# Kernel tuning notes

Measured on AMD Instinct MI355X. Metric: run time of the kernel, lower is better.

## Reference

```python
import jax, jax.numpy as jnp
import numpy as np
import math

B, TH, STEPS = 4, 120, 8
D_IN, D_MODEL, N_HEADS, N_LAYERS, D_FF = 32, 512, 8, 4, 2048
N_SUB = 5
D_HEAD = D_MODEL // N_HEADS
EPS = 1e-5


def _pos_encoding(T, d):
    pos = jnp.arange(T, dtype=jnp.float32)[:, None]
    div = jnp.exp(jnp.arange(0, d, 2, dtype=jnp.float32) * (-math.log(10000.0) / d))
    pe = jnp.zeros((T, d), dtype=jnp.float32)
    pe = pe.at[:, 0::2].set(jnp.sin(pos * div))
    pe = pe.at[:, 1::2].set(jnp.cos(pos * div))
    return pe


def setup_inputs() -> dict:
    key = jax.random.key(0)
    ks = jax.random.split(key, 16)
    s = 0.02
    n = lambda k, shp: jax.random.normal(k, shp, jnp.float32) * s
    return {
        "history": jax.random.normal(ks[0], (B, TH, D_IN), jnp.float32),
        "steps": STEPS,
        "W_emb": n(ks[1], (D_MODEL, D_IN)),
        "b_emb": jnp.zeros((D_MODEL,), jnp.float32),
        "Wq": n(ks[2], (N_LAYERS, D_MODEL, D_MODEL)),
        "Wk": n(ks[3], (N_LAYERS, D_MODEL, D_MODEL)),
        "Wv": n(ks[4], (N_LAYERS, D_MODEL, D_MODEL)),
        "Wo": n(ks[5], (N_LAYERS, D_MODEL, D_MODEL)),
        "ln1_g": jnp.ones((N_LAYERS, D_MODEL), jnp.float32),
        "ln1_b": jnp.zeros((N_LAYERS, D_MODEL), jnp.float32),
        "W1": n(ks[6], (N_LAYERS, D_FF, D_MODEL)),
        "b1": jnp.zeros((N_LAYERS, D_FF), jnp.float32),
        "W2": n(ks[7], (N_LAYERS, D_MODEL, D_FF)),
        "b2": jnp.zeros((N_LAYERS, D_MODEL), jnp.float32),
        "ln2_g": jnp.ones((N_LAYERS, D_MODEL), jnp.float32),
        "ln2_b": jnp.zeros((N_LAYERS, D_MODEL), jnp.float32),
        "Wr1": n(ks[8], (D_FF, 2 * D_MODEL)),
        "br1": jnp.zeros((D_FF,), jnp.float32),
        "Wr2": n(ks[9], (D_IN, D_FF)),
        "br2": jnp.zeros((D_IN,), jnp.float32),
    }


def _layernorm(x, g, b):
    mu = x.mean(-1, keepdims=True)
    var = ((x - mu) ** 2).mean(-1, keepdims=True)
    return (x - mu) / jnp.sqrt(var + EPS) * g + b


def reference(history, steps, W_emb, b_emb, Wq, Wk, Wv, Wo, ln1_g, ln1_b,
              W1, b1, W2, b2, ln2_g, ln2_b, Wr1, br1, Wr2, br2):
    total_len = TH + steps
    pe = _pos_encoding(total_len, D_MODEL)
    idx = jnp.arange(total_len)
    # NOTE: faithful to source: mask True where kv index > q index (equinox: True = attend)
    mask = idx[:, None] < idx[None, :]
    neg = jnp.finfo(jnp.float32).min
    scale = math.sqrt(D_MODEL)

    def transformer(buf):  # buf: [T, D_IN] -> [T, D_MODEL]
        h = (buf @ W_emb.T + b_emb) * scale + pe
        for l in range(N_LAYERS):
            q = (h @ Wq[l].T).reshape(total_len, N_HEADS, D_HEAD)
            k = (h @ Wk[l].T).reshape(total_len, N_HEADS, D_HEAD)
            v = (h @ Wv[l].T).reshape(total_len, N_HEADS, D_HEAD)
            logits = jnp.einsum("qhd,khd->hqk", q, k) / math.sqrt(D_HEAD)
            logits = jnp.where(mask[None], logits, neg)
            w = jax.nn.softmax(logits, axis=-1)
            attn = jnp.einsum("hqk,khd->qhd", w, v).reshape(total_len, D_MODEL)
            h = _layernorm(h + attn @ Wo[l].T, ln1_g[l], ln1_b[l])
            m = jax.nn.gelu(h @ W1[l].T + b1[l]) @ W2[l].T + b2[l]
            h = _layernorm(h + m, ln2_g[l], ln2_b[l])
        return h

    def refine(start_val, ctx):  # start_val: [D_IN], ctx: [D_MODEL]
        def body(i, cur):
            we = (W_emb @ cur + b_emb) * scale
            comb = jnp.concatenate([we, ctx])
            delta = Wr2 @ jax.nn.gelu(Wr1 @ comb + br1) + br2
            return cur + delta
        return jax.lax.fori_loop(0, N_SUB, body, start_val)

    def single(hist):  # [TH, D_IN] -> [steps, D_IN]
        buf = jnp.zeros((total_len, D_IN), jnp.float32).at[:TH].set(hist)

        def scan_fn(buf, step_idx):
            h = transformer(buf)  # full recompute each decode step (no KV cache)
            ptr = TH + step_idx
            next_val = refine(buf[ptr - 1], h[ptr - 1])
            return buf.at[ptr].set(next_val), next_val

        _, preds = jax.lax.scan(scan_fn, buf, jnp.arange(steps))
        return preds

    return jax.vmap(single)(history)
```

## Files before the change

kernel.cpp:

```cpp
#include <hip/hip_runtime.h>
#include <math.h>

namespace {
constexpr int NB = 4;
constexpr int SEQ = 128;
constexpr int TH_ = 120;
constexpr int NSTEP = 8;
constexpr int DMODEL = 512;
constexpr int NHEAD = 8;
constexpr int DHEAD = 64;
constexpr int DFFN = 2048;
constexpr int DIN = 32;
constexpr int MROWS = NB*SEQ;
constexpr float SCALE_EMB = 22.627416997969522f;
constexpr float LN_EPS = 1e-5f;
constexpr float NEGF = -3.4028234663852886e38f;
constexpr float PE_C = -0.017988946039015984f;
}

using short8 = __attribute__((ext_vector_type(8))) short;
using f32x4  = __attribute__((ext_vector_type(4))) float;

__device__ __forceinline__ float wave_sum(float v){
#pragma unroll
  for(int off=32;off;off>>=1) v += __shfl_xor(v,off,64);
  return v;
}
__device__ __forceinline__ float blk_sum(float v, float* scr){
  v = wave_sum(v);
  __syncthreads();
  if((threadIdx.x&63)==0) scr[threadIdx.x>>6]=v;
  __syncthreads();
  return scr[0]+scr[1]+scr[2]+scr[3];
}
__device__ __forceinline__ float gelu_t(float x){
  float t = 0.7978845608028654f*(x + 0.044715f*x*x*x);
  return 0.5f*x*(1.0f + tanhf(t));
}
__device__ __forceinline__ float pe_val(int t, int d){
  float div = expf((float)(d & ~1) * PE_C);
  float a = (float)t * div;
  return (d & 1) ? cosf(a) : sinf(a);
}
__device__ __forceinline__ unsigned short f2b(float f){
  union { float f; unsigned u; } c; c.f = f;
  unsigned u = c.u + 0x7FFFu + ((c.u>>16)&1u);
  return (unsigned short)(u>>16);
}
__device__ __forceinline__ short8 pack8(const float* f){
  short8 s;
#pragma unroll
  for(int i=0;i<8;i++) s[i] = (short)f2b(f[i]);
  return s;
}

__global__ __launch_bounds__(256) void conv_w(const float* __restrict__ Wq,
                                              const float* __restrict__ Wk,
                                              const float* __restrict__ Wv,
                                              const float* __restrict__ Wo,
                                              const float* __restrict__ W1,
                                              const float* __restrict__ W2,
                                              unsigned short* __restrict__ dst){
  size_t base = ((size_t)blockIdx.x*256 + threadIdx.x)*8;
  if(base >= 12582912u) return;
  const float* src; size_t off;
  if(base < 1048576u){ src=Wq; off=base; }
  else if(base < 2097152u){ src=Wk; off=base-1048576u; }
  else if(base < 3145728u){ src=Wv; off=base-2097152u; }
  else if(base < 4194304u){ src=Wo; off=base-3145728u; }
  else if(base < 8388608u){ src=W1; off=base-4194304u; }
  else { src=W2; off=base-8388608u; }
  float4 a = *(const float4*)(src+off);
  float4 b = *(const float4*)(src+off+4);
  float f[8] = {a.x,a.y,a.z,a.w,b.x,b.y,b.z,b.w};
  *(short8*)(dst + base) = pack8(f);
}

__global__ __launch_bounds__(256) void init_h0(const float* __restrict__ hist,
                                               const float* __restrict__ W_emb,
                                               const float* __restrict__ b_emb,
                                               float* __restrict__ h0,
                                               unsigned short* __restrict__ h0b){
  int bt = blockIdx.x;
  int b = bt >> 7, t = bt & 127;
  __shared__ float x[DIN];
  if(threadIdx.x < DIN)
    x[threadIdx.x] = (t < TH_) ? hist[((size_t)b*TH_ + t)*DIN + threadIdx.x] : 0.f;
  __syncthreads();
  for(int d = threadIdx.x; d < DMODEL; d += 256){
    float s = 0.f;
#pragma unroll 8
    for(int i=0;i<DIN;i++) s += W_emb[d*DIN+i]*x[i];
    float v = SCALE_EMB*(s + b_emb[d]) + pe_val(t,d);
    h0[(size_t)bt*DMODEL + d] = v;
    h0b[(size_t)bt*DMODEL + d] = f2b(v);
  }
}

__global__ __launch_bounds__(256) void init_misc(const float* __restrict__ Wr1,
                                                 const float* __restrict__ W_emb,
                                                 const float* __restrict__ b_emb,
                                                 const float* __restrict__ br1,
                                                 const float* __restrict__ hist,
                                                 float* __restrict__ M1,
                                                 float* __restrict__ cb1,
                                                 float* __restrict__ cur_x){
  __shared__ float row[DMODEL];
  int j0 = blockIdx.x*8;
  for(int jj=0;jj<8;jj++){
    int j = j0+jj;
    for(int k=threadIdx.x;k<DMODEL;k+=256) row[k] = Wr1[(size_t)j*1024 + k];
    __syncthreads();
    if(threadIdx.x < DIN){
      int i = threadIdx.x; float s = 0.f;
      for(int k=0;k<DMODEL;k++) s += row[k]*W_emb[k*DIN+i];
      M1[j*DIN+i] = SCALE_EMB*s;
    } else if(threadIdx.x == DIN){
      float s=0.f;
      for(int k=0;k<DMODEL;k++) s += row[k]*b_emb[k];
      cb1[j] = br1[j] + SCALE_EMB*s;
    }
    __syncthreads();
  }
  if(blockIdx.x==0 && threadIdx.x<NB*DIN){
    int b = threadIdx.x>>5, i = threadIdx.x&31;
    cur_x[b*DIN+i] = hist[((size_t)b*TH_ + (TH_-1))*DIN + i];
  }
}

__global__ __launch_bounds__(256) void lnpass(const float* __restrict__ X,
                                              const float* __restrict__ g,
                                              const float* __restrict__ bta,
                                              float* __restrict__ Y,
                                              unsigned short* __restrict__ Yb){
  int row = blockIdx.x*4 + (threadIdx.x>>6);
  int l = threadIdx.x&63;
  const float* xp = X + (size_t)row*DMODEL + l*8;
  float4 x0 = *(const float4*)xp;
  float4 x1 = *(const float4*)(xp+4);
  float f[8] = {x0.x,x0.y,x0.z,x0.w,x1.x,x1.y,x1.z,x1.w};
  float s = 0.f;
#pragma unroll
  for(int i=0;i<8;i++) s += f[i];
  s = wave_sum(s);
  float mu = s*(1.f/DMODEL);
  float v = 0.f;
#pragma unroll
  for(int i=0;i<8;i++){ float d0=f[i]-mu; v += d0*d0; }
  v = wave_sum(v);
  float rs = rsqrtf(v*(1.f/DMODEL) + LN_EPS);
#pragma unroll
  for(int i=0;i<8;i++){
    int c = l*8+i;
    f[i] = (f[i]-mu)*rs*g[c] + bta[c];
  }
  float* yp = Y + (size_t)row*DMODEL + l*8;
  *(float4*)yp     = make_float4(f[0],f[1],f[2],f[3]);
  *(float4*)(yp+4) = make_float4(f[4],f[5],f[6],f[7]);
  *(short8*)(Yb + (size_t)row*DMODEL + l*8) = pack8(f);
}

__global__ __launch_bounds__(256) void gemm_bf(
    const unsigned short* __restrict__ A16, int Ka,
    const unsigned short* __restrict__ Wa,
    const unsigned short* __restrict__ Wb,
    const unsigned short* __restrict__ Wc,
    const float* __restrict__ bias, const float* __restrict__ resid,
    float* __restrict__ Cf, unsigned short* __restrict__ Cb,
    int c_rs, int c_mode, int act)
{
  int n0 = blockIdx.x*128;
  int m0 = blockIdx.y*64;
  int tid = threadIdx.x, w = tid>>6, ln = tid&63;
  __shared__ __align__(16) unsigned short As[64][72];
  __shared__ __align__(16) unsigned short Bs[128][72];

  const unsigned short* Wsrc; int nrow0;
  if(c_mode==2){ int which = n0>>9; Wsrc = (which==0?Wa:(which==1?Wb:Wc)); nrow0 = n0&511; }
  else { Wsrc = Wa; nrow0 = n0; }

  f32x4 acc[4][2];
#pragma unroll
  for(int i=0;i<4;i++)
#pragma unroll
    for(int j=0;j<2;j++) acc[i][j] = (f32x4){0.f,0.f,0.f,0.f};

  int fr = ln&15, fq = (ln>>4)*8;
  int arow = tid>>2, akq = (tid&3)*16;
  int brow = tid>>1, bkq = (tid&1)*32;

  for(int k0=0;k0<Ka;k0+=64){
    const unsigned short* ap = A16 + (size_t)(m0+arow)*Ka + k0 + akq;
    short8 a0 = *(const short8*)ap;
    short8 a1 = *(const short8*)(ap+8);
    const unsigned short* bp = Wsrc + (size_t)(nrow0+brow)*Ka + k0 + bkq;
    short8 b0 = *(const short8*)bp;
    short8 b1 = *(const short8*)(bp+8);
    short8 b2 = *(const short8*)(bp+16);
    short8 b3 = *(const short8*)(bp+24);
    *(short8*)&As[arow][akq]   = a0;
    *(short8*)&As[arow][akq+8] = a1;
    *(short8*)&Bs[brow][bkq]    = b0;
    *(short8*)&Bs[brow][bkq+8]  = b1;
    *(short8*)&Bs[brow][bkq+16] = b2;
    *(short8*)&Bs[brow][bkq+24] = b3;
    __syncthreads();
    short8 af[4][2], bf[2][2];
#pragma unroll
    for(int kf=0;kf<2;kf++){
#pragma unroll
      for(int rt=0;rt<4;rt++) af[rt][kf] = *(const short8*)&As[rt*16 + fr][kf*32 + fq];
#pragma unroll
      for(int ct=0;ct<2;ct++) bf[ct][kf] = *(const short8*)&Bs[32*w + ct*16 + fr][kf*32 + fq];
    }
#pragma unroll
    for(int kf=0;kf<2;kf++)
#pragma unroll
      for(int rt=0;rt<4;rt++)
#pragma unroll
        for(int ct=0;ct<2;ct++)
          acc[rt][ct] = __builtin_amdgcn_mfma_f32_16x16x32_bf16(af[rt][kf], bf[ct][kf], acc[rt][ct], 0, 0, 0);
    __syncthreads();
  }

#pragma unroll
  for(int rt=0;rt<4;rt++){
#pragma unroll
    for(int ct=0;ct<2;ct++){
      int n = n0 + 32*w + ct*16 + fr;
#pragma unroll
      for(int r=0;r<4;r++){
        int row = m0 + rt*16 + (ln>>4)*4 + r;
        float v = acc[rt][ct][r];
        if(bias)  v += bias[n];
        if(resid) v += resid[(size_t)row*DMODEL + n];
        if(act==1) v = gelu_t(v);
        if(c_mode==0)      Cf[(size_t)row*c_rs + n] = v;
        else if(c_mode==1) Cb[(size_t)row*c_rs + n] = f2b(v);
        else {
          int which = n>>9, rem = n&511;
          int b = row>>7, t = row&127;
          Cf[(size_t)which*(MROWS*DMODEL) +
             ((size_t)(b*NHEAD + (rem>>6))*SEQ + t)*DHEAD + (rem&63)] = v;
        }
      }
    }
  }
}

__global__ __launch_bounds__(256) void attn_k(const float* __restrict__ qb,
                                              const float* __restrict__ kb,
                                              const float* __restrict__ vb,
                                              unsigned short* __restrict__ attb){
  int b = blockIdx.z, h = blockIdx.y;
  int r0 = blockIdx.x*32;
  const float* Kh = kb + (size_t)(b*NHEAD+h)*SEQ*DHEAD;
  const float* Vh = vb + (size_t)(b*NHEAD+h)*SEQ*DHEAD;
  const float* Qh = qb + (size_t)(b*NHEAD+h)*SEQ*DHEAD;
  __shared__ float kv[SEQ][DHEAD];
  __shared__ float wsm[32][132];
  __shared__ float qs[32][68];
  int tid = threadIdx.x;
  int d = tid&63, rr = tid>>6;

  for(int k=rr;k<SEQ;k+=4) kv[k][d ^ (k&60)] = Kh[k*DHEAD + d];
  for(int r=rr;r<32;r+=4)  qs[r][d] = Qh[(size_t)(r0+r)*DHEAD + d];
  __syncthreads();

  {
    int rp = tid>>4;
    int kg = tid&15;
    float acc[2][8];
#pragma unroll
    for(int i=0;i<2;i++)
#pragma unroll
      for(int kk=0;kk<8;kk++) acc[i][kk]=0.f;
#pragma unroll 4
    for(int d4=0;d4<16;d4++){
      float4 q0 = *(const float4*)&qs[2*rp][d4*4];
      float4 q1 = *(const float4*)&qs[2*rp+1][d4*4];
#pragma unroll
      for(int kk=0;kk<8;kk++){
        int k = 8*kg + kk;
        int off = (d4*4) ^ (k&60);
        float4 kv4 = *(const float4*)&kv[k][off];
        acc[0][kk] += q0.x*kv4.x + q0.y*kv4.y + q0.z*kv4.z + q0.w*kv4.w;
        acc[1][kk] += q1.x*kv4.x + q1.y*kv4.y + q1.z*kv4.z + q1.w*kv4.w;
      }
    }
#pragma unroll
    for(int i=0;i<2;i++){
      int t = r0 + 2*rp + i;
#pragma unroll
      for(int kk=0;kk<8;kk++){
        int k = 8*kg + kk;
        wsm[2*rp+i][k] = (k > t) ? acc[i][kk]*0.125f : NEGF;
      }
    }
  }
  __syncthreads();

  {
    int l2 = tid&63, wv = tid>>6;
    for(int r=wv;r<32;r+=4){
      float l0 = wsm[r][l2], l1 = wsm[r][l2+64];
      float m = fmaxf(l0,l1);
#pragma unroll
      for(int off=32;off;off>>=1) m = fmaxf(m, __shfl_xor(m,off,64));
      float e0 = expf(l0-m), e1 = expf(l1-m);
      float s = e0+e1;
      s = wave_sum(s);
      float inv = 1.f/s;
      wsm[r][l2] = e0*inv; wsm[r][l2+64] = e1*inv;
    }
  }
  __syncthreads();

  for(int k=rr;k<SEQ;k+=4) kv[k][d] = Vh[k*DHEAD + d];
  __syncthreads();

  {
    int dq = (tid&15)*4, rg = tid>>4;
    for(int r=rg;r<32;r+=16){
      float4 acc2 = make_float4(0.f,0.f,0.f,0.f);
      for(int k=0;k<SEQ;k++){
        float w0 = wsm[r][k];
        float4 v = *(const float4*)&kv[k][dq];
        acc2.x += w0*v.x; acc2.y += w0*v.y; acc2.z += w0*v.z; acc2.w += w0*v.w;
      }
      int row = b*SEQ + r0 + r;
      unsigned short* op = attb + (size_t)row*DMODEL + h*DHEAD + dq;
      op[0]=f2b(acc2.x); op[1]=f2b(acc2.y); op[2]=f2b(acc2.z); op[3]=f2b(acc2.w);
    }
  }
}

__global__ __launch_bounds__(256) void ctx_k(const float* __restrict__ r2,
                                             const float* __restrict__ g2,
                                             const float* __restrict__ b2,
                                             const float* __restrict__ Wr1,
                                             const float* __restrict__ cb1,
                                             float* __restrict__ ctxt, int ptr){
  int b = blockIdx.y; int j0 = blockIdx.x*128;
  __shared__ float raw[DMODEL], ctx[DMODEL], scr[4];
  int tid = threadIdx.x;
  const float* rp = r2 + (size_t)(b*SEQ + ptr-1)*DMODEL;
  for(int k=tid;k<DMODEL;k+=256) raw[k]=rp[k];
  __syncthreads();
  float s = 0.f;
  for(int k=tid;k<DMODEL;k+=256) s += raw[k];
  s = blk_sum(s, scr);
  float mu = s/(float)DMODEL;
  float v = 0.f;
  for(int k=tid;k<DMODEL;k+=256){ float d0 = raw[k]-mu; v += d0*d0; }
  v = blk_sum(v, scr);
  float rs = rsqrtf(v/(float)DMODEL + LN_EPS);
  for(int k=tid;k<DMODEL;k+=256) ctx[k] = (raw[k]-mu)*rs*g2[k] + b2[k];
  __syncthreads();
  int wv = tid>>6, l2 = tid&63;
  for(int jj=wv;jj<128;jj+=4){
    int j = j0+jj;
    const float* wp = Wr1 + (size_t)j*1024 + 512;
    float acc = 0.f;
#pragma unroll
    for(int q=0;q<8;q++){ int k = l2 + 64*q; acc += wp[k]*ctx[k]; }
    acc = wave_sum(acc);
    if(l2==0) ctxt[b*DFFN + j] = acc + cb1[j];
  }
}

__global__ __launch_bounds__(256) void refine_fin(const float* __restrict__ M1,
                                                  const float* __restrict__ ctxt,
                                                  const float* __restrict__ Wr2,
                                                  const float* __restrict__ br2,
                                                  float* __restrict__ cur_x,
                                                  const float* __restrict__ W_emb,
                                                  const float* __restrict__ b_emb,
                                                  float* __restrict__ out,
                                                  float* __restrict__ h0,
                                                  unsigned short* __restrict__ h0b,
                                                  int s, int ptr){
  int b = blockIdx.x, tid = threadIdx.x;
  __shared__ float cur[DIN], gs[DFFN], dscr[DIN];
  if(tid < DIN) cur[tid] = cur_x[b*DIN + tid];
  __syncthreads();
  for(int sub=0; sub<5; sub++){
    for(int jj=tid; jj<DFFN; jj+=256){
      float u = ctxt[b*DFFN + jj];
      const float* mp = M1 + (size_t)jj*DIN;
#pragma unroll
      for(int p=0;p<8;p++){
        float4 mv = *(const float4*)(mp + 4*p);
        u += mv.x*cur[4*p] + mv.y*cur[4*p+1] + mv.z*cur[4*p+2] + mv.w*cur[4*p+3];
      }
      gs[jj] = gelu_t(u);
    }
    __syncthreads();
    int w = tid>>6, l = tid&63;
#pragma unroll
    for(int q=0;q<8;q++){
      int i = w*8 + q;
      const float* wr = Wr2 + (size_t)i*DFFN;
      float a = 0.f;
#pragma unroll
      for(int p=0;p<8;p++){
        int j0 = p*256 + l*4;
        float4 wv = *(const float4*)(wr + j0);
        float4 gv = *(const float4*)&gs[j0];
        a += wv.x*gv.x + wv.y*gv.y + wv.z*gv.z + wv.w*gv.w;
      }
      a = wave_sum(a);
      if(l==0) dscr[i] = a;
    }
    __syncthreads();
    if(tid < DIN) cur[tid] += dscr[tid] + br2[tid];
    __syncthreads();
  }
  if(tid < DIN){
    out[(b*NSTEP + s)*DIN + tid] = cur[tid];
    cur_x[b*DIN + tid] = cur[tid];
  }
  __syncthreads();
  for(int d=tid; d<DMODEL; d+=256){
    float s2 = 0.f;
#pragma unroll 8
    for(int i=0;i<DIN;i++) s2 += W_emb[d*DIN+i]*cur[i];
    float v = SCALE_EMB*(s2 + b_emb[d]) + pe_val(ptr, d);
    size_t idx = (size_t)(b*SEQ + ptr)*DMODEL + d;
    h0[idx] = v;
    h0b[idx] = f2b(v);
  }
}

extern "C" void kernel_launch(void* const* d_in, const int* in_sizes, int n_in,
                              void* d_out, int out_size, void* d_ws, size_t ws_size,
                              hipStream_t stream) {
  (void)in_sizes; (void)n_in; (void)out_size; (void)ws_size;
  const float* hist = (const float*)d_in[0];
  const float* W_emb= (const float*)d_in[2];
  const float* b_emb= (const float*)d_in[3];
  const float* Wq   = (const float*)d_in[4];
  const float* Wk   = (const float*)d_in[5];
  const float* Wv   = (const float*)d_in[6];
  const float* Wo   = (const float*)d_in[7];
  const float* ln1g = (const float*)d_in[8];
  const float* ln1b = (const float*)d_in[9];
  const float* W1   = (const float*)d_in[10];
  const float* b1   = (const float*)d_in[11];
  const float* W2   = (const float*)d_in[12];
  const float* b2v  = (const float*)d_in[13];
  const float* ln2g = (const float*)d_in[14];
  const float* ln2b = (const float*)d_in[15];
  const float* Wr1  = (const float*)d_in[16];
  const float* br1  = (const float*)d_in[17];
  const float* Wr2  = (const float*)d_in[18];
  const float* br2  = (const float*)d_in[19];
  float* out = (float*)d_out;
  float* ws  = (float*)d_ws;

  const size_t BTD = (size_t)MROWS*DMODEL;
  const size_t BTDH = BTD/2;
  float* h0   = ws;
  unsigned short* h0b = (unsigned short*)(h0 + BTD);
  float* r2   = h0 + BTD + BTDH;
  float* hln  = r2 + BTD;
  float* hp   = hln + BTD;
  unsigned short* hpb = (unsigned short*)(hp + BTD);
  float* qb   = hp + BTD + BTDH;
  float* kb   = qb + BTD;
  float* vb   = kb + BTD;
  unsigned short* attb = (unsigned short*)(vb + BTD);
  unsigned short* hlnb = (unsigned short*)(vb + BTD + BTDH);
  unsigned short* fbuf16 = (unsigned short*)qb;
  float* r1   = qb;
  unsigned short* W16 = (unsigned short*)(qb + 4*BTD);
  float* after_w = qb + 4*BTD + 6291456;
  float* M1   = after_w;
  float* cb1  = M1 + (size_t)DFFN*DIN;
  float* ctxt = cb1 + DFFN;
  float* cur_x= ctxt + NB*DFFN;

  unsigned short* Wq16 = W16;
  unsigned short* Wk16 = W16 + 1048576;
  unsigned short* Wv16 = W16 + 2097152;
  unsigned short* Wo16 = W16 + 3145728;
  unsigned short* W116 = W16 + 4194304;
  unsigned short* W216 = W16 + 8388608;

  conv_w<<<dim3(6144),dim3(256),0,stream>>>(Wq,Wk,Wv,Wo,W1,W2,W16);
  init_h0<<<dim3(MROWS),dim3(256),0,stream>>>(hist,W_emb,b_emb,h0,h0b);
  init_misc<<<dim3(256),dim3(256),0,stream>>>(Wr1,W_emb,b_emb,br1,hist,M1,cb1,cur_x);

  for(int s=0;s<NSTEP;s++){
    int ptr = TH_ + s;
    for(int l=0;l<4;l++){
      if(l>0)
        lnpass<<<dim3(128),dim3(256),0,stream>>>(r2, ln2g+(l-1)*DMODEL, ln2b+(l-1)*DMODEL, hln, hlnb);
      const unsigned short* A16 = (l==0)? h0b : hlnb;
      const float* res1 = (l==0)? h0 : hln;

      gemm_bf<<<dim3(12,8),dim3(256),0,stream>>>(A16, DMODEL,
          Wq16 + (size_t)l*262144, Wk16 + (size_t)l*262144, Wv16 + (size_t)l*262144,
          nullptr, nullptr, qb, nullptr, 0, 2, 0);

      attn_k<<<dim3(4,NHEAD,NB),dim3(256),0,stream>>>(qb,kb,vb,attb);

      gemm_bf<<<dim3(4,8),dim3(256),0,stream>>>(attb, DMODEL,
          Wo16 + (size_t)l*262144, nullptr, nullptr,
          nullptr, res1, r1, nullptr, DMODEL, 0, 0);

      lnpass<<<dim3(128),dim3(256),0,stream>>>(r1, ln1g+l*DMODEL, ln1b+l*DMODEL, hp, hpb);

      gemm_bf<<<dim3(16,8),dim3(256),0,stream>>>(hpb, DMODEL,
          W116 + (size_t)l*1048576, nullptr, nullptr,
          b1 + l*DFFN, nullptr, nullptr, fbuf16, DFFN, 1, 1);

      gemm_bf<<<dim3(4,8),dim3(256),0,stream>>>(fbuf16, DFFN,
          W216 + (size_t)l*1048576, nullptr, nullptr,
          b2v + l*DMODEL, hp, r2, nullptr, DMODEL, 0, 0);
    }

    ctx_k<<<dim3(16,NB),dim3(256),0,stream>>>(r2, ln2g + 3*DMODEL, ln2b + 3*DMODEL,
                                              Wr1, cb1, ctxt, ptr);
    refine_fin<<<dim3(NB),dim3(256),0,stream>>>(M1, ctxt, Wr2, br2, cur_x,
                                                W_emb, b_emb, out, h0, h0b, s, ptr);
  }
}
```

Measured before the change: 4.746 ms.

## Fuse per-step decode kernels into one persistent kernel with grid barriers

Replaces the roughly 230 small kernel launches of the decode loop with a single persistent 128-block kernel. Stages are separated by an atomic-counter grid barrier, and the stage bodies share one shared-memory union. The aim is to remove launch overhead and inter-kernel gaps. In exchange, every stage runs on at most 128 blocks, so some stages leave blocks idle, and the spin barrier assumes all blocks are co-resident.

```diff
diff --git a/kernel.cpp b/kernel.cpp
--- a/kernel.cpp
+++ b/kernel.cpp
@@ -16,10 +16,13 @@
 constexpr float LN_EPS = 1e-5f;
 constexpr float NEGF = -3.4028234663852886e38f;
 constexpr float PE_C = -0.017988946039015984f;
+constexpr unsigned NBLK = 128;
 }
 
 using short8 = __attribute__((ext_vector_type(8))) short;
 using f32x4  = __attribute__((ext_vector_type(4))) float;
+
+__device__ unsigned g_cnt = 0;
 
 __device__ __forceinline__ float wave_sum(float v){
 #pragma unroll
@@ -53,6 +56,23 @@
   for(int i=0;i<8;i++) s[i] = (short)f2b(f[i]);
   return s;
 }
+
+__device__ __forceinline__ void gsync(unsigned target){
+  __syncthreads();
+  if(threadIdx.x==0){
+    __hip_atomic_fetch_add(&g_cnt, 1u, __ATOMIC_ACQ_REL, __HIP_MEMORY_SCOPE_AGENT);
+    while(__hip_atomic_load(&g_cnt, __ATOMIC_ACQUIRE, __HIP_MEMORY_SCOPE_AGENT) < target){
+      __builtin_amdgcn_s_sleep(1);
+    }
+  }
+  __syncthreads();
+}
+
+struct SmemG { unsigned short As[64][72]; unsigned short Bs[128][72]; };
+struct SmemA { float kv[SEQ][DHEAD]; float wsm[32][132]; float qs[32][68]; };
+struct SmemC { float raw[DMODEL]; float ctx[DMODEL]; float scr[4]; };
+struct SmemR { float cur[DIN]; float gs[DFFN]; float dscr[DIN]; };
+union alignas(16) SmemU { SmemG g; SmemA a; SmemC c; SmemR r; };
 
 __global__ __launch_bounds__(256) void conv_w(const float* __restrict__ Wq,
                                               const float* __restrict__ Wk,
@@ -105,6 +125,7 @@
                                                  float* __restrict__ M1,
                                                  float* __restrict__ cb1,
                                                  float* __restrict__ cur_x){
+  if(blockIdx.x==0 && threadIdx.x==255) g_cnt = 0u;
   __shared__ float row[DMODEL];
   int j0 = blockIdx.x*8;
   for(int jj=0;jj<8;jj++){
@@ -128,12 +149,14 @@
   }
 }
 
-__global__ __launch_bounds__(256) void lnpass(const float* __restrict__ X,
-                                              const float* __restrict__ g,
-                                              const float* __restrict__ bta,
-                                              float* __restrict__ Y,
-                                              unsigned short* __restrict__ Yb){
-  int row = blockIdx.x*4 + (threadIdx.x>>6);
+
+__device__ __forceinline__ void lnpass_body(int vb,
+                                            const float* __restrict__ X,
+                                            const float* __restrict__ g,
+                                            const float* __restrict__ bta,
+                                            float* __restrict__ Y,
+                                            unsigned short* __restrict__ Yb){
+  int row = vb*4 + (threadIdx.x>>6);
   int l = threadIdx.x&63;
   const float* xp = X + (size_t)row*DMODEL + l*8;
   float4 x0 = *(const float4*)xp;
@@ -160,7 +183,7 @@
   *(short8*)(Yb + (size_t)row*DMODEL + l*8) = pack8(f);
 }
 
-__global__ __launch_bounds__(256) void gemm_bf(
+__device__ __forceinline__ void gemm_body(int bx, int by, SmemG& S,
     const unsigned short* __restrict__ A16, int Ka,
     const unsigned short* __restrict__ Wa,
     const unsigned short* __restrict__ Wb,
@@ -169,11 +192,9 @@
     float* __restrict__ Cf, unsigned short* __restrict__ Cb,
     int c_rs, int c_mode, int act)
 {
-  int n0 = blockIdx.x*128;
-  int m0 = blockIdx.y*64;
+  int n0 = bx*128;
+  int m0 = by*64;
   int tid = threadIdx.x, w = tid>>6, ln = tid&63;
-  __shared__ __align__(16) unsigned short As[64][72];
-  __shared__ __align__(16) unsigned short Bs[128][72];
 
   const unsigned short* Wsrc; int nrow0;
   if(c_mode==2){ int which = n0>>9; Wsrc = (which==0?Wa:(which==1?Wb:Wc)); nrow0 = n0&511; }
@@ -198,20 +219,20 @@
     short8 b1 = *(const short8*)(bp+8);
     short8 b2 = *(const short8*)(bp+16);
     short8 b3 = *(const short8*)(bp+24);
-    *(short8*)&As[arow][akq]   = a0;
-    *(short8*)&As[arow][akq+8] = a1;
-    *(short8*)&Bs[brow][bkq]    = b0;
-    *(short8*)&Bs[brow][bkq+8]  = b1;
-    *(short8*)&Bs[brow][bkq+16] = b2;
-    *(short8*)&Bs[brow][bkq+24] = b3;
+    *(short8*)&S.As[arow][akq]   = a0;
+    *(short8*)&S.As[arow][akq+8] = a1;
+    *(short8*)&S.Bs[brow][bkq]    = b0;
+    *(short8*)&S.Bs[brow][bkq+8]  = b1;
+    *(short8*)&S.Bs[brow][bkq+16] = b2;
+    *(short8*)&S.Bs[brow][bkq+24] = b3;
     __syncthreads();
     short8 af[4][2], bf[2][2];
 #pragma unroll
     for(int kf=0;kf<2;kf++){
 #pragma unroll
-      for(int rt=0;rt<4;rt++) af[rt][kf] = *(const short8*)&As[rt*16 + fr][kf*32 + fq];
-#pragma unroll
-      for(int ct=0;ct<2;ct++) bf[ct][kf] = *(const short8*)&Bs[32*w + ct*16 + fr][kf*32 + fq];
+      for(int rt=0;rt<4;rt++) af[rt][kf] = *(const short8*)&S.As[rt*16 + fr][kf*32 + fq];
+#pragma unroll
+      for(int ct=0;ct<2;ct++) bf[ct][kf] = *(const short8*)&S.Bs[32*w + ct*16 + fr][kf*32 + fq];
     }
 #pragma unroll
     for(int kf=0;kf<2;kf++)
@@ -248,23 +269,20 @@
   }
 }
 
-__global__ __launch_bounds__(256) void attn_k(const float* __restrict__ qb,
-                                              const float* __restrict__ kb,
-                                              const float* __restrict__ vb,
-                                              unsigned short* __restrict__ attb){
-  int b = blockIdx.z, h = blockIdx.y;
-  int r0 = blockIdx.x*32;
-  const float* Kh = kb + (size_t)(b*NHEAD+h)*SEQ*DHEAD;
-  const float* Vh = vb + (size_t)(b*NHEAD+h)*SEQ*DHEAD;
-  const float* Qh = qb + (size_t)(b*NHEAD+h)*SEQ*DHEAD;
-  __shared__ float kv[SEQ][DHEAD];
-  __shared__ float wsm[32][132];
-  __shared__ float qs[32][68];
+__device__ __forceinline__ void attn_body(int bx, int h, int b, SmemA& S,
+                                          const float* __restrict__ qb,
+                                          const float* __restrict__ kb,
+                                          const float* __restrict__ vbuf,
+                                          unsigned short* __restrict__ attb){
+  int r0 = bx*32;
+  const float* Kh = kb   + (size_t)(b*NHEAD+h)*SEQ*DHEAD;
+  const float* Vh = vbuf + (size_t)(b*NHEAD+h)*SEQ*DHEAD;
+  const float* Qh = qb   + (size_t)(b*NHEAD+h)*SEQ*DHEAD;
   int tid = threadIdx.x;
   int d = tid&63, rr = tid>>6;
 
-  for(int k=rr;k<SEQ;k+=4) kv[k][d ^ (k&60)] = Kh[k*DHEAD + d];
-  for(int r=rr;r<32;r+=4)  qs[r][d] = Qh[(size_t)(r0+r)*DHEAD + d];
+  for(int k=rr;k<SEQ;k+=4) S.kv[k][d ^ (k&60)] = Kh[k*DHEAD + d];
+  for(int r=rr;r<32;r+=4)  S.qs[r][d] = Qh[(size_t)(r0+r)*DHEAD + d];
   __syncthreads();
 
   {
@@ -277,13 +295,13 @@
       for(int kk=0;kk<8;kk++) acc[i][kk]=0.f;
 #pragma unroll 4
     for(int d4=0;d4<16;d4++){
-      float4 q0 = *(const float4*)&qs[2*rp][d4*4];
-      float4 q1 = *(const float4*)&qs[2*rp+1][d4*4];
+      float4 q0 = *(const float4*)&S.qs[2*rp][d4*4];
+      float4 q1 = *(const float4*)&S.qs[2*rp+1][d4*4];
 #pragma unroll
       for(int kk=0;kk<8;kk++){
         int k = 8*kg + kk;
         int off = (d4*4) ^ (k&60);
-        float4 kv4 = *(const float4*)&kv[k][off];
+        float4 kv4 = *(const float4*)&S.kv[k][off];
         acc[0][kk] += q0.x*kv4.x + q0.y*kv4.y + q0.z*kv4.z + q0.w*kv4.w;
         acc[1][kk] += q1.x*kv4.x + q1.y*kv4.y + q1.z*kv4.z + q1.w*kv4.w;
       }
@@ -294,7 +312,7 @@
 #pragma unroll
       for(int kk=0;kk<8;kk++){
         int k = 8*kg + kk;
-        wsm[2*rp+i][k] = (k > t) ? acc[i][kk]*0.125f : NEGF;
+        S.wsm[2*rp+i][k] = (k > t) ? acc[i][kk]*0.125f : NEGF;
       }
     }
   }
@@ -303,7 +321,7 @@
   {
     int l2 = tid&63, wv = tid>>6;
     for(int r=wv;r<32;r+=4){
-      float l0 = wsm[r][l2], l1 = wsm[r][l2+64];
+      float l0 = S.wsm[r][l2], l1 = S.wsm[r][l2+64];
       float m = fmaxf(l0,l1);
 #pragma unroll
       for(int off=32;off;off>>=1) m = fmaxf(m, __shfl_xor(m,off,64));
@@ -311,12 +329,12 @@
       float s = e0+e1;
       s = wave_sum(s);
       float inv = 1.f/s;
-      wsm[r][l2] = e0*inv; wsm[r][l2+64] = e1*inv;
-    }
-  }
-  __syncthreads();
-
-  for(int k=rr;k<SEQ;k+=4) kv[k][d] = Vh[k*DHEAD + d];
+      S.wsm[r][l2] = e0*inv; S.wsm[r][l2+64] = e1*inv;
+    }
+  }
+  __syncthreads();
+
+  for(int k=rr;k<SEQ;k+=4) S.kv[k][d] = Vh[k*DHEAD + d];
   __syncthreads();
 
   {
@@ -324,8 +342,8 @@
     for(int r=rg;r<32;r+=16){
       float4 acc2 = make_float4(0.f,0.f,0.f,0.f);
       for(int k=0;k<SEQ;k++){
-        float w0 = wsm[r][k];
-        float4 v = *(const float4*)&kv[k][dq];
+        float w0 = S.wsm[r][k];
+        float4 v = *(const float4*)&S.kv[k][dq];
         acc2.x += w0*v.x; acc2.y += w0*v.y; acc2.z += w0*v.z; acc2.w += w0*v.w;
       }
       int row = b*SEQ + r0 + r;
@@ -335,27 +353,27 @@
   }
 }
 
-__global__ __launch_bounds__(256) void ctx_k(const float* __restrict__ r2,
-                                             const float* __restrict__ g2,
-                                             const float* __restrict__ b2,
-                                             const float* __restrict__ Wr1,
-                                             const float* __restrict__ cb1,
-                                             float* __restrict__ ctxt, int ptr){
-  int b = blockIdx.y; int j0 = blockIdx.x*128;
-  __shared__ float raw[DMODEL], ctx[DMODEL], scr[4];
+__device__ __forceinline__ void ctx_body(int jx, int b, SmemC& S,
+                                         const float* __restrict__ r2,
+                                         const float* __restrict__ g2,
+                                         const float* __restrict__ b2,
+                                         const float* __restrict__ Wr1,
+                                         const float* __restrict__ cb1,
+                                         float* __restrict__ ctxt, int ptr){
+  int j0 = jx*128;
   int tid = threadIdx.x;
   const float* rp = r2 + (size_t)(b*SEQ + ptr-1)*DMODEL;
-  for(int k=tid;k<DMODEL;k+=256) raw[k]=rp[k];
+  for(int k=tid;k<DMODEL;k+=256) S.raw[k]=rp[k];
   __syncthreads();
   float s = 0.f;
-  for(int k=tid;k<DMODEL;k+=256) s += raw[k];
-  s = blk_sum(s, scr);
+  for(int k=tid;k<DMODEL;k+=256) s += S.raw[k];
+  s = blk_sum(s, S.scr);
   float mu = s/(float)DMODEL;
   float v = 0.f;
-  for(int k=tid;k<DMODEL;k+=256){ float d0 = raw[k]-mu; v += d0*d0; }
-  v = blk_sum(v, scr);
+  for(int k=tid;k<DMODEL;k+=256){ float d0 = S.raw[k]-mu; v += d0*d0; }
+  v = blk_sum(v, S.scr);
   float rs = rsqrtf(v/(float)DMODEL + LN_EPS);
-  for(int k=tid;k<DMODEL;k+=256) ctx[k] = (raw[k]-mu)*rs*g2[k] + b2[k];
+  for(int k=tid;k<DMODEL;k+=256) S.ctx[k] = (S.raw[k]-mu)*rs*g2[k] + b2[k];
   __syncthreads();
   int wv = tid>>6, l2 = tid&63;
   for(int jj=wv;jj<128;jj+=4){
@@ -363,26 +381,26 @@
     const float* wp = Wr1 + (size_t)j*1024 + 512;
     float acc = 0.f;
 #pragma unroll
-    for(int q=0;q<8;q++){ int k = l2 + 64*q; acc += wp[k]*ctx[k]; }
+    for(int q=0;q<8;q++){ int k = l2 + 64*q; acc += wp[k]*S.ctx[k]; }
     acc = wave_sum(acc);
     if(l2==0) ctxt[b*DFFN + j] = acc + cb1[j];
   }
 }
 
-__global__ __launch_bounds__(256) void refine_fin(const float* __restrict__ M1,
-                                                  const float* __restrict__ ctxt,
-                                                  const float* __restrict__ Wr2,
-                                                  const float* __restrict__ br2,
-                                                  float* __restrict__ cur_x,
-                                                  const float* __restrict__ W_emb,
-                                                  const float* __restrict__ b_emb,
-                                                  float* __restrict__ out,
-                                                  float* __restrict__ h0,
-                                                  unsigned short* __restrict__ h0b,
-                                                  int s, int ptr){
-  int b = blockIdx.x, tid = threadIdx.x;
-  __shared__ float cur[DIN], gs[DFFN], dscr[DIN];
-  if(tid < DIN) cur[tid] = cur_x[b*DIN + tid];
+__device__ __forceinline__ void refine_body(int b, SmemR& S,
+                                            const float* __restrict__ M1,
+                                            const float* __restrict__ ctxt,
+                                            const float* __restrict__ Wr2,
+                                            const float* __restrict__ br2,
+                                            float* __restrict__ cur_x,
+                                            const float* __restrict__ W_emb,
+                                            const float* __restrict__ b_emb,
+                                            float* __restrict__ out,
+                                            float* __restrict__ h0,
+                                            unsigned short* __restrict__ h0b,
+                                            int s, int ptr){
+  int tid = threadIdx.x;
+  if(tid < DIN) S.cur[tid] = cur_x[b*DIN + tid];
   __syncthreads();
   for(int sub=0; sub<5; sub++){
     for(int jj=tid; jj<DFFN; jj+=256){
@@ -391,9 +409,9 @@
 #pragma unroll
       for(int p=0;p<8;p++){
         float4 mv = *(const float4*)(mp + 4*p);
-        u += mv.x*cur[4*p] + mv.y*cur[4*p+1] + mv.z*cur[4*p+2] + mv.w*cur[4*p+3];
+        u += mv.x*S.cur[4*p] + mv.y*S.cur[4*p+1] + mv.z*S.cur[4*p+2] + mv.w*S.cur[4*p+3];
       }
-      gs[jj] = gelu_t(u);
+      S.gs[jj] = gelu_t(u);
     }
     __syncthreads();
     int w = tid>>6, l = tid&63;
@@ -406,30 +424,100 @@
       for(int p=0;p<8;p++){
         int j0 = p*256 + l*4;
         float4 wv = *(const float4*)(wr + j0);
-        float4 gv = *(const float4*)&gs[j0];
+        float4 gv = *(const float4*)&S.gs[j0];
         a += wv.x*gv.x + wv.y*gv.y + wv.z*gv.z + wv.w*gv.w;
       }
       a = wave_sum(a);
-      if(l==0) dscr[i] = a;
-    }
-    __syncthreads();
-    if(tid < DIN) cur[tid] += dscr[tid] + br2[tid];
+      if(l==0) S.dscr[i] = a;
+    }
+    __syncthreads();
+    if(tid < DIN) S.cur[tid] += S.dscr[tid] + br2[tid];
     __syncthreads();
   }
   if(tid < DIN){
-    out[(b*NSTEP + s)*DIN + tid] = cur[tid];
-    cur_x[b*DIN + tid] = cur[tid];
+    out[(b*NSTEP + s)*DIN + tid] = S.cur[tid];
+    cur_x[b*DIN + tid] = S.cur[tid];
   }
   __syncthreads();
   for(int d=tid; d<DMODEL; d+=256){
     float s2 = 0.f;
 #pragma unroll 8
-    for(int i=0;i<DIN;i++) s2 += W_emb[d*DIN+i]*cur[i];
+    for(int i=0;i<DIN;i++) s2 += W_emb[d*DIN+i]*S.cur[i];
     float v = SCALE_EMB*(s2 + b_emb[d]) + pe_val(ptr, d);
     size_t idx = (size_t)(b*SEQ + ptr)*DMODEL + d;
     h0[idx] = v;
     h0b[idx] = f2b(v);
   }
+}
+
+struct MegaP {
+  const float *ln1g, *ln1b, *b1, *b2v, *ln2g, *ln2b, *Wr1, *W_emb, *b_emb, *Wr2, *br2;
+  float *out;
+  float *h0; unsigned short *h0b;
+  float *r2, *hln, *hp; unsigned short *hpb;
+  float *qb, *kb, *vb; unsigned short *attb, *hlnb, *fbuf16;
+  float *r1;
+  const unsigned short *Wq16, *Wk16, *Wv16, *Wo16, *W116, *W216;
+  float *M1, *cb1, *ctxt, *cur_x;
+};
+
+__global__ __launch_bounds__(256,1) void mega(MegaP p){
+  __shared__ SmemU sm;
+  const unsigned vbk = blockIdx.x;
+  unsigned ep = 0;
+#define GS() do{ ++ep; gsync(ep*NBLK); }while(0)
+
+  for(int s=0;s<NSTEP;s++){
+    int ptr = TH_ + s;
+    for(int l=0;l<4;l++){
+      const unsigned short* A16; const float* res1;
+      if(l>0){
+        lnpass_body(vbk, p.r2, p.ln2g+(l-1)*DMODEL, p.ln2b+(l-1)*DMODEL, p.hln, p.hlnb);
+        GS();
+        A16 = p.hlnb; res1 = p.hln;
+      } else { A16 = p.h0b; res1 = p.h0; }
+
+      if(vbk < 96)
+        gemm_body((int)(vbk%12u), (int)(vbk/12u), sm.g, A16, DMODEL,
+                  p.Wq16 + (size_t)l*262144, p.Wk16 + (size_t)l*262144, p.Wv16 + (size_t)l*262144,
+                  nullptr, nullptr, p.qb, nullptr, 0, 2, 0);
+      GS();
+
+      attn_body((int)(vbk&3u), (int)((vbk>>2)&7u), (int)(vbk>>5), sm.a, p.qb, p.kb, p.vb, p.attb);
+      GS();
+
+      if(vbk < 32)
+        gemm_body((int)(vbk&3u), (int)(vbk>>2), sm.g, p.attb, DMODEL,
+                  p.Wo16 + (size_t)l*262144, nullptr, nullptr,
+                  nullptr, res1, p.r1, nullptr, DMODEL, 0, 0);
+      GS();
+
+      lnpass_body(vbk, p.r1, p.ln1g+l*DMODEL, p.ln1b+l*DMODEL, p.hp, p.hpb);
+      GS();
+
+      gemm_body((int)(vbk&15u), (int)(vbk>>4), sm.g, p.hpb, DMODEL,
+                p.W116 + (size_t)l*1048576, nullptr, nullptr,
+                p.b1 + l*DFFN, nullptr, nullptr, p.fbuf16, DFFN, 1, 1);
+      GS();
+
+      if(vbk < 32)
+        gemm_body((int)(vbk&3u), (int)(vbk>>2), sm.g, p.fbuf16, DFFN,
+                  p.W216 + (size_t)l*1048576, nullptr, nullptr,
+                  p.b2v + l*DMODEL, p.hp, p.r2, nullptr, DMODEL, 0, 0);
+      GS();
+    }
+
+    if(vbk < 64)
+      ctx_body((int)(vbk&15u), (int)(vbk>>4), sm.c, p.r2,
+               p.ln2g + 3*DMODEL, p.ln2b + 3*DMODEL, p.Wr1, p.cb1, p.ctxt, ptr);
+    GS();
+
+    if(vbk < 4)
+      refine_body((int)vbk, sm.r, p.M1, p.ctxt, p.Wr2, p.br2, p.cur_x,
+                  p.W_emb, p.b_emb, p.out, p.h0, p.h0b, s, ptr);
+    GS();
+  }
+#undef GS
 }
 
 extern "C" void kernel_launch(void* const* d_in, const int* in_sizes, int n_in,
@@ -491,38 +579,16 @@
   init_h0<<<dim3(MROWS),dim3(256),0,stream>>>(hist,W_emb,b_emb,h0,h0b);
   init_misc<<<dim3(256),dim3(256),0,stream>>>(Wr1,W_emb,b_emb,br1,hist,M1,cb1,cur_x);
 
-  for(int s=0;s<NSTEP;s++){
-    int ptr = TH_ + s;
-    for(int l=0;l<4;l++){
-      if(l>0)
-        lnpass<<<dim3(128),dim3(256),0,stream>>>(r2, ln2g+(l-1)*DMODEL, ln2b+(l-1)*DMODEL, hln, hlnb);
-      const unsigned short* A16 = (l==0)? h0b : hlnb;
-      const float* res1 = (l==0)? h0 : hln;
-
-      gemm_bf<<<dim3(12,8),dim3(256),0,stream>>>(A16, DMODEL,
-          Wq16 + (size_t)l*262144, Wk16 + (size_t)l*262144, Wv16 + (size_t)l*262144,
-          nullptr, nullptr, qb, nullptr, 0, 2, 0);
-
-      attn_k<<<dim3(4,NHEAD,NB),dim3(256),0,stream>>>(qb,kb,vb,attb);
-
-      gemm_bf<<<dim3(4,8),dim3(256),0,stream>>>(attb, DMODEL,
-          Wo16 + (size_t)l*262144, nullptr, nullptr,
-          nullptr, res1, r1, nullptr, DMODEL, 0, 0);
-
-      lnpass<<<dim3(128),dim3(256),0,stream>>>(r1, ln1g+l*DMODEL, ln1b+l*DMODEL, hp, hpb);
-
-      gemm_bf<<<dim3(16,8),dim3(256),0,stream>>>(hpb, DMODEL,
-          W116 + (size_t)l*1048576, nullptr, nullptr,
-          b1 + l*DFFN, nullptr, nullptr, fbuf16, DFFN, 1, 1);
-
-      gemm_bf<<<dim3(4,8),dim3(256),0,stream>>>(fbuf16, DFFN,
-          W216 + (size_t)l*1048576, nullptr, nullptr,
-          b2v + l*DMODEL, hp, r2, nullptr, DMODEL, 0, 0);
-    }
-
-    ctx_k<<<dim3(16,NB),dim3(256),0,stream>>>(r2, ln2g + 3*DMODEL, ln2b + 3*DMODEL,
-                                              Wr1, cb1, ctxt, ptr);
-    refine_fin<<<dim3(NB),dim3(256),0,stream>>>(M1, ctxt, Wr2, br2, cur_x,
-                                                W_emb, b_emb, out, h0, h0b, s, ptr);
-  }
-}
+  MegaP p;
+  p.ln1g=ln1g; p.ln1b=ln1b; p.b1=b1; p.b2v=b2v; p.ln2g=ln2g; p.ln2b=ln2b;
+  p.Wr1=Wr1; p.W_emb=W_emb; p.b_emb=b_emb; p.Wr2=Wr2; p.br2=br2;
+  p.out=out;
+  p.h0=h0; p.h0b=h0b;
+  p.r2=r2; p.hln=hln; p.hp=hp; p.hpb=hpb;
+  p.qb=qb; p.kb=kb; p.vb=vb; p.attb=attb; p.hlnb=hlnb; p.fbuf16=fbuf16;
+  p.r1=r1;
+  p.Wq16=Wq16; p.Wk16=Wk16; p.Wv16=Wv16; p.Wo16=Wo16; p.W116=W116; p.W216=W216;
+  p.M1=M1; p.cb1=cb1; p.ctxt=ctxt; p.cur_x=cur_x;
+
+  mega<<<dim3(NBLK),dim3(256),0,stream>>>(p);
+}
```

Result: slower. 11.36 ms (+139.4%).

## Fuse layernorm passes into GEMM prologues/epilogues and prefetch GEMM tiles

Applied to the files above, without the earlier changes.

Removes the standalone lnpass kernels. LayerNorm is now applied inside the GEMMs: on the A-operand load for the QKV and FFN1 GEMMs, and on the residual term in the epilogue for the Wo and FFN2 GEMMs. Each GEMM block recomputes per-row mean and variance for its 64 rows. The GEMM also register-prefetches the next K tile before computing on the current one. Attention loads K, Q and V with float4 vector loads. This saves launches and intermediate buffer traffic at the cost of redundant statistics work across N-blocks.

```diff
diff --git a/kernel.cpp b/kernel.cpp
--- a/kernel.cpp
+++ b/kernel.cpp
@@ -128,57 +128,62 @@
   }
 }
 
-__global__ __launch_bounds__(256) void lnpass(const float* __restrict__ X,
-                                              const float* __restrict__ g,
-                                              const float* __restrict__ bta,
-                                              float* __restrict__ Y,
-                                              unsigned short* __restrict__ Yb){
-  int row = blockIdx.x*4 + (threadIdx.x>>6);
-  int l = threadIdx.x&63;
-  const float* xp = X + (size_t)row*DMODEL + l*8;
-  float4 x0 = *(const float4*)xp;
-  float4 x1 = *(const float4*)(xp+4);
-  float f[8] = {x0.x,x0.y,x0.z,x0.w,x1.x,x1.y,x1.z,x1.w};
-  float s = 0.f;
-#pragma unroll
-  for(int i=0;i<8;i++) s += f[i];
-  s = wave_sum(s);
-  float mu = s*(1.f/DMODEL);
-  float v = 0.f;
-#pragma unroll
-  for(int i=0;i<8;i++){ float d0=f[i]-mu; v += d0*d0; }
-  v = wave_sum(v);
-  float rs = rsqrtf(v*(1.f/DMODEL) + LN_EPS);
-#pragma unroll
-  for(int i=0;i<8;i++){
-    int c = l*8+i;
-    f[i] = (f[i]-mu)*rs*g[c] + bta[c];
-  }
-  float* yp = Y + (size_t)row*DMODEL + l*8;
-  *(float4*)yp     = make_float4(f[0],f[1],f[2],f[3]);
-  *(float4*)(yp+4) = make_float4(f[4],f[5],f[6],f[7]);
-  *(short8*)(Yb + (size_t)row*DMODEL + l*8) = pack8(f);
-}
-
-__global__ __launch_bounds__(256) void gemm_bf(
+template<int LNM>
+__global__ __launch_bounds__(256,1) void gemm_k(
     const unsigned short* __restrict__ A16, int Ka,
     const unsigned short* __restrict__ Wa,
     const unsigned short* __restrict__ Wb,
     const unsigned short* __restrict__ Wc,
     const float* __restrict__ bias, const float* __restrict__ resid,
+    const float* __restrict__ lnx, const float* __restrict__ lng,
+    const float* __restrict__ lnbta,
     float* __restrict__ Cf, unsigned short* __restrict__ Cb,
     int c_rs, int c_mode, int act)
 {
-  int n0 = blockIdx.x*128;
-  int m0 = blockIdx.y*64;
-  int tid = threadIdx.x, w = tid>>6, ln = tid&63;
   __shared__ __align__(16) unsigned short As[64][72];
   __shared__ __align__(16) unsigned short Bs[128][72];
+  __shared__ float Smu[64], Srs[64];
+  __shared__ float Sgs[DMODEL], Scs[DMODEL];
+
+  int bx = blockIdx.x, by = blockIdx.y;
+  int n0 = bx*128;
+  int m0 = by*64;
+  int tid = threadIdx.x, w = tid>>6, ln = tid&63;
 
   const unsigned short* Wsrc; int nrow0;
   if(c_mode==2){ int which = n0>>9; Wsrc = (which==0?Wa:(which==1?Wb:Wc)); nrow0 = n0&511; }
   else { Wsrc = Wa; nrow0 = n0; }
 
+  if constexpr(LNM != 0){
+    float4 xr[16][2];
+#pragma unroll
+    for(int rr=0;rr<16;rr++){
+      const float* xp = lnx + (size_t)(m0 + w*16 + rr)*DMODEL + ln*8;
+      xr[rr][0] = *(const float4*)xp;
+      xr[rr][1] = *(const float4*)(xp+4);
+    }
+    if constexpr(LNM==1){
+      for(int k=tid;k<DMODEL;k+=256){ Sgs[k]=lng[k]; Scs[k]=lnbta[k]; }
+    }
+#pragma unroll
+    for(int rr=0;rr<16;rr++){
+      float f[8] = {xr[rr][0].x,xr[rr][0].y,xr[rr][0].z,xr[rr][0].w,
+                    xr[rr][1].x,xr[rr][1].y,xr[rr][1].z,xr[rr][1].w};
+      float s = 0.f;
+#pragma unroll
+      for(int i=0;i<8;i++) s += f[i];
+      s = wave_sum(s);
+      float mu = s*(1.f/DMODEL);
+      float v2 = 0.f;
+#pragma unroll
+      for(int i=0;i<8;i++){ float d0=f[i]-mu; v2 += d0*d0; }
+      v2 = wave_sum(v2);
+      float rsv = rsqrtf(v2*(1.f/DMODEL) + LN_EPS);
+      if(ln==0){ Smu[w*16+rr]=mu; Srs[w*16+rr]=rsv; }
+    }
+    __syncthreads();
+  }
+
   f32x4 acc[4][2];
 #pragma unroll
   for(int i=0;i<4;i++)
@@ -189,22 +194,57 @@
   int arow = tid>>2, akq = (tid&3)*16;
   int brow = tid>>1, bkq = (tid&1)*32;
 
+  float amu=0.f, ars=0.f;
+  if constexpr(LNM==1){ amu = Smu[arow]; ars = Srs[arow]; }
+
+  short8 a0, a1;
+  float4 t0, t1, t2, t3;
+  short8 b0, b1, b2, b3;
+
+  auto LOADB = [&](int k0){
+    const unsigned short* bp = Wsrc + (size_t)(nrow0+brow)*Ka + k0 + bkq;
+    b0 = *(const short8*)bp;
+    b1 = *(const short8*)(bp+8);
+    b2 = *(const short8*)(bp+16);
+    b3 = *(const short8*)(bp+24);
+  };
+  auto LOADA = [&](int k0){
+    if constexpr(LNM==1){
+      const float* fp = lnx + (size_t)(m0+arow)*DMODEL + k0 + akq;
+      t0 = *(const float4*)fp;
+      t1 = *(const float4*)(fp+4);
+      t2 = *(const float4*)(fp+8);
+      t3 = *(const float4*)(fp+12);
+    } else {
+      const unsigned short* ap = A16 + (size_t)(m0+arow)*Ka + k0 + akq;
+      a0 = *(const short8*)ap;
+      a1 = *(const short8*)(ap+8);
+    }
+  };
+
+  LOADA(0); LOADB(0);
   for(int k0=0;k0<Ka;k0+=64){
-    const unsigned short* ap = A16 + (size_t)(m0+arow)*Ka + k0 + akq;
-    short8 a0 = *(const short8*)ap;
-    short8 a1 = *(const short8*)(ap+8);
-    const unsigned short* bp = Wsrc + (size_t)(nrow0+brow)*Ka + k0 + bkq;
-    short8 b0 = *(const short8*)bp;
-    short8 b1 = *(const short8*)(bp+8);
-    short8 b2 = *(const short8*)(bp+16);
-    short8 b3 = *(const short8*)(bp+24);
-    *(short8*)&As[arow][akq]   = a0;
-    *(short8*)&As[arow][akq+8] = a1;
+    if constexpr(LNM==1){
+      float tt[16] = {t0.x,t0.y,t0.z,t0.w, t1.x,t1.y,t1.z,t1.w,
+                      t2.x,t2.y,t2.z,t2.w, t3.x,t3.y,t3.z,t3.w};
+      float o[16];
+#pragma unroll
+      for(int i=0;i<16;i++){
+        int c = k0 + akq + i;
+        o[i] = (tt[i]-amu)*ars*Sgs[c] + Scs[c];
+      }
+      *(short8*)&As[arow][akq]   = pack8(o);
+      *(short8*)&As[arow][akq+8] = pack8(o+8);
+    } else {
+      *(short8*)&As[arow][akq]   = a0;
+      *(short8*)&As[arow][akq+8] = a1;
+    }
     *(short8*)&Bs[brow][bkq]    = b0;
     *(short8*)&Bs[brow][bkq+8]  = b1;
     *(short8*)&Bs[brow][bkq+16] = b2;
     *(short8*)&Bs[brow][bkq+24] = b3;
     __syncthreads();
+    if(k0+64 < Ka){ LOADA(k0+64); LOADB(k0+64); }
     short8 af[4][2], bf[2][2];
 #pragma unroll
     for(int kf=0;kf<2;kf++){
@@ -223,17 +263,39 @@
     __syncthreads();
   }
 
+  float rv[4][2][4];
+  const float* rsrc = (LNM==2) ? lnx : resid;
+  if(rsrc){
+#pragma unroll
+    for(int rt=0;rt<4;rt++)
+#pragma unroll
+      for(int ct=0;ct<2;ct++){
+        int n = n0 + 32*w + ct*16 + fr;
+        int row0 = m0 + rt*16 + (ln>>4)*4;
+        const float* p = rsrc + (size_t)row0*DMODEL + n;
+#pragma unroll
+        for(int r=0;r<4;r++) rv[rt][ct][r] = p[(size_t)r*DMODEL];
+      }
+  }
+
 #pragma unroll
   for(int rt=0;rt<4;rt++){
 #pragma unroll
     for(int ct=0;ct<2;ct++){
       int n = n0 + 32*w + ct*16 + fr;
+      int ri0 = rt*16 + (ln>>4)*4;
+      int row0 = m0 + ri0;
 #pragma unroll
       for(int r=0;r<4;r++){
-        int row = m0 + rt*16 + (ln>>4)*4 + r;
+        int ri = ri0 + r;
+        int row = row0 + r;
         float v = acc[rt][ct][r];
         if(bias)  v += bias[n];
-        if(resid) v += resid[(size_t)row*DMODEL + n];
+        if constexpr(LNM==2){
+          v += (rv[rt][ct][r] - Smu[ri])*Srs[ri]*lng[n] + lnbta[n];
+        } else {
+          if(rsrc) v += rv[rt][ct][r];
+        }
         if(act==1) v = gelu_t(v);
         if(c_mode==0)      Cf[(size_t)row*c_rs + n] = v;
         else if(c_mode==1) Cb[(size_t)row*c_rs + n] = f2b(v);
@@ -261,10 +323,19 @@
   __shared__ float wsm[32][132];
   __shared__ float qs[32][68];
   int tid = threadIdx.x;
-  int d = tid&63, rr = tid>>6;
-
-  for(int k=rr;k<SEQ;k+=4) kv[k][d ^ (k&60)] = Kh[k*DHEAD + d];
-  for(int r=rr;r<32;r+=4)  qs[r][d] = Qh[(size_t)(r0+r)*DHEAD + d];
+  int kk = tid>>4, d4 = (tid&15)*4;
+
+  {
+    float4 t[8];
+#pragma unroll
+    for(int i=0;i<8;i++) t[i] = *(const float4*)(Kh + (size_t)(kk+16*i)*DHEAD + d4);
+    float4 q0 = *(const float4*)(Qh + (size_t)(r0+kk)*DHEAD + d4);
+    float4 q1 = *(const float4*)(Qh + (size_t)(r0+kk+16)*DHEAD + d4);
+#pragma unroll
+    for(int i=0;i<8;i++){ int k = kk+16*i; *(float4*)&kv[k][d4 ^ (k&60)] = t[i]; }
+    *(float4*)&qs[kk   ][d4] = q0;
+    *(float4*)&qs[kk+16][d4] = q1;
+  }
   __syncthreads();
 
   {
@@ -274,27 +345,27 @@
 #pragma unroll
     for(int i=0;i<2;i++)
 #pragma unroll
-      for(int kk=0;kk<8;kk++) acc[i][kk]=0.f;
+      for(int kk2=0;kk2<8;kk2++) acc[i][kk2]=0.f;
 #pragma unroll 4
-    for(int d4=0;d4<16;d4++){
-      float4 q0 = *(const float4*)&qs[2*rp][d4*4];
-      float4 q1 = *(const float4*)&qs[2*rp+1][d4*4];
-#pragma unroll
-      for(int kk=0;kk<8;kk++){
-        int k = 8*kg + kk;
-        int off = (d4*4) ^ (k&60);
+    for(int dd=0;dd<16;dd++){
+      float4 q0 = *(const float4*)&qs[2*rp][dd*4];
+      float4 q1 = *(const float4*)&qs[2*rp+1][dd*4];
+#pragma unroll
+      for(int kk2=0;kk2<8;kk2++){
+        int k = 8*kg + kk2;
+        int off = (dd*4) ^ (k&60);
         float4 kv4 = *(const float4*)&kv[k][off];
-        acc[0][kk] += q0.x*kv4.x + q0.y*kv4.y + q0.z*kv4.z + q0.w*kv4.w;
-        acc[1][kk] += q1.x*kv4.x + q1.y*kv4.y + q1.z*kv4.z + q1.w*kv4.w;
+        acc[0][kk2] += q0.x*kv4.x + q0.y*kv4.y + q0.z*kv4.z + q0.w*kv4.w;
+        acc[1][kk2] += q1.x*kv4.x + q1.y*kv4.y + q1.z*kv4.z + q1.w*kv4.w;
       }
     }
 #pragma unroll
     for(int i=0;i<2;i++){
       int t = r0 + 2*rp + i;
 #pragma unroll
-      for(int kk=0;kk<8;kk++){
-        int k = 8*kg + kk;
-        wsm[2*rp+i][k] = (k > t) ? acc[i][kk]*0.125f : NEGF;
+      for(int kk2=0;kk2<8;kk2++){
+        int k = 8*kg + kk2;
+        wsm[2*rp+i][k] = (k > t) ? acc[i][kk2]*0.125f : NEGF;
       }
     }
   }
@@ -316,7 +387,13 @@
   }
   __syncthreads();
 
-  for(int k=rr;k<SEQ;k+=4) kv[k][d] = Vh[k*DHEAD + d];
+  {
+    float4 t[8];
+#pragma unroll
+    for(int i=0;i<8;i++) t[i] = *(const float4*)(Vh + (size_t)(kk+16*i)*DHEAD + d4);
+#pragma unroll
+    for(int i=0;i<8;i++) *(float4*)&kv[kk+16*i][d4] = t[i];
+  }
   __syncthreads();
 
   {
@@ -465,14 +542,12 @@
   float* r2   = h0 + BTD + BTDH;
   float* hln  = r2 + BTD;
   float* hp   = hln + BTD;
-  unsigned short* hpb = (unsigned short*)(hp + BTD);
   float* qb   = hp + BTD + BTDH;
   float* kb   = qb + BTD;
   float* vb   = kb + BTD;
   unsigned short* attb = (unsigned short*)(vb + BTD);
-  unsigned short* hlnb = (unsigned short*)(vb + BTD + BTDH);
   unsigned short* fbuf16 = (unsigned short*)qb;
-  float* r1   = qb;
+  float* r1   = hp;
   unsigned short* W16 = (unsigned short*)(qb + 4*BTD);
   float* after_w = qb + 4*BTD + 6291456;
   float* M1   = after_w;
@@ -494,30 +569,44 @@
   for(int s=0;s<NSTEP;s++){
     int ptr = TH_ + s;
     for(int l=0;l<4;l++){
-      if(l>0)
-        lnpass<<<dim3(128),dim3(256),0,stream>>>(r2, ln2g+(l-1)*DMODEL, ln2b+(l-1)*DMODEL, hln, hlnb);
-      const unsigned short* A16 = (l==0)? h0b : hlnb;
-      const float* res1 = (l==0)? h0 : hln;
-
-      gemm_bf<<<dim3(12,8),dim3(256),0,stream>>>(A16, DMODEL,
-          Wq16 + (size_t)l*262144, Wk16 + (size_t)l*262144, Wv16 + (size_t)l*262144,
-          nullptr, nullptr, qb, nullptr, 0, 2, 0);
+      const float* g2p = ln2g + (l-1)*DMODEL;
+      const float* b2p = ln2b + (l-1)*DMODEL;
+      const float* g1p = ln1g + l*DMODEL;
+      const float* b1p = ln1b + l*DMODEL;
+
+      if(l==0)
+        gemm_k<0><<<dim3(12,8),dim3(256),0,stream>>>(h0b, DMODEL,
+            Wq16 + (size_t)l*262144, Wk16 + (size_t)l*262144, Wv16 + (size_t)l*262144,
+            nullptr, nullptr, nullptr, nullptr, nullptr,
+            qb, nullptr, 0, 2, 0);
+      else
+        gemm_k<1><<<dim3(12,8),dim3(256),0,stream>>>(nullptr, DMODEL,
+            Wq16 + (size_t)l*262144, Wk16 + (size_t)l*262144, Wv16 + (size_t)l*262144,
+            nullptr, nullptr, r2, g2p, b2p,
+            qb, nullptr, 0, 2, 0);
 
       attn_k<<<dim3(4,NHEAD,NB),dim3(256),0,stream>>>(qb,kb,vb,attb);
 
-      gemm_bf<<<dim3(4,8),dim3(256),0,stream>>>(attb, DMODEL,
-          Wo16 + (size_t)l*262144, nullptr, nullptr,
-          nullptr, res1, r1, nullptr, DMODEL, 0, 0);
-
-      lnpass<<<dim3(128),dim3(256),0,stream>>>(r1, ln1g+l*DMODEL, ln1b+l*DMODEL, hp, hpb);
-
-      gemm_bf<<<dim3(16,8),dim3(256),0,stream>>>(hpb, DMODEL,
+      if(l==0)
+        gemm_k<0><<<dim3(4,8),dim3(256),0,stream>>>(attb, DMODEL,
+            Wo16 + (size_t)l*262144, nullptr, nullptr,
+            nullptr, h0, nullptr, nullptr, nullptr,
+            r1, nullptr, DMODEL, 0, 0);
+      else
+        gemm_k<2><<<dim3(4,8),dim3(256),0,stream>>>(attb, DMODEL,
+            Wo16 + (size_t)l*262144, nullptr, nullptr,
+            nullptr, nullptr, r2, g2p, b2p,
+            r1, nullptr, DMODEL, 0, 0);
+
+      gemm_k<1><<<dim3(16,8),dim3(256),0,stream>>>(nullptr, DMODEL,
           W116 + (size_t)l*1048576, nullptr, nullptr,
-          b1 + l*DFFN, nullptr, nullptr, fbuf16, DFFN, 1, 1);
-
-      gemm_bf<<<dim3(4,8),dim3(256),0,stream>>>(fbuf16, DFFN,
+          b1 + l*DFFN, nullptr, r1, g1p, b1p,
+          nullptr, fbuf16, DFFN, 1, 1);
+
+      gemm_k<2><<<dim3(4,8),dim3(256),0,stream>>>(fbuf16, DFFN,
           W216 + (size_t)l*1048576, nullptr, nullptr,
-          b2v + l*DMODEL, hp, r2, nullptr, DMODEL, 0, 0);
+          b2v + l*DMODEL, nullptr, r1, g1p, b1p,
+          r2, nullptr, DMODEL, 0, 0);
     }
 
     ctx_k<<<dim3(16,NB),dim3(256),0,stream>>>(r2, ln2g + 3*DMODEL, ln2b + 3*DMODEL,
```

Measured after the change: 4.996 ms. 1.05x slower.
